# Kernel tuning notes

Hardware: AMD Instinct MI355X
Metric: run time of the kernel (lower is better)

The kernel has to match this reference:

```python
import jax, jax.numpy as jnp
import numpy as np

B, TQ, TV, D, U = 16, 64, 256, 512, 512

def setup_inputs() -> dict:
    key = jax.random.key(0)
    ks = jax.random.split(key, 9)
    s = 1.0 / np.sqrt(D)
    return {
        "query": jax.random.normal(ks[0], (B, TQ, D), dtype=jnp.float32),
        "values": jax.random.normal(ks[1], (B, TV, D), dtype=jnp.float32),
        "enc_mask": jax.random.randint(ks[2], (B, TV), 0, 2, dtype=jnp.int32),
        "W1": jax.random.normal(ks[3], (D, U), dtype=jnp.float32) * s,
        "b1": jnp.zeros((U,), dtype=jnp.float32),
        "W2": jax.random.normal(ks[4], (D, U), dtype=jnp.float32) * s,
        "b2": jnp.zeros((U,), dtype=jnp.float32),
        "Vw": jax.random.normal(ks[5], (U,), dtype=jnp.float32) * (1.0 / np.sqrt(U)),
        "Vb": jnp.zeros((), dtype=jnp.float32),
    }

def reference(query, values, enc_mask, W1, b1, W2, b2, Vw, Vb):
    # q_proj: [B,Tq,U]; v_proj: [B,Tv,U]
    q_proj = jnp.einsum("bqd,du->bqu", query, W1) + b1
    v_proj = jnp.einsum("bvd,du->bvu", values, W2) + b2
    # broadcast add -> [B,Tq,Tv,U], tanh, project to scalar score [B,Tq,Tv]
    s = jnp.tanh(q_proj[:, :, None, :] + v_proj[:, None, :, :])
    score = jnp.einsum("bqvu,u->bqv", s, Vw) + Vb
    # additive mask over encoder positions (mask[1] in the original call)
    score = score - (1.0 - enc_mask.astype(score.dtype))[:, None, :] * 1e9
    attn_weights = jax.nn.softmax(score, axis=2)  # [B,Tq,Tv]
    context = jnp.einsum("bqv,bvd->bqd", attn_weights, values)
    return (context, attn_weights)
```

## Files before the change

### kernel.cpp

```cpp
#include <hip/hip_runtime.h>

#define NB  16
#define NTQ 64
#define NTV 256
#define ND  512
#define NU  512

typedef _Float16 half8_t __attribute__((ext_vector_type(8)));
typedef _Float16 half4_t __attribute__((ext_vector_type(4)));
typedef _Float16 half2_t __attribute__((ext_vector_type(2)));
typedef float floatx4 __attribute__((ext_vector_type(4)));

#if __has_builtin(__builtin_amdgcn_fdot2)
#define FDOT2(a, b, c) __builtin_amdgcn_fdot2((a), (b), (c), false)
#else
#define FDOT2(a, b, c) ((c) + (float)((a)[0]) * (float)((b)[0]) + (float)((a)[1]) * (float)((b)[1]))
#endif
#if __has_builtin(__builtin_amdgcn_rcph)
#define RCPH(x) ((_Float16)__builtin_amdgcn_rcph((_Float16)(x)))
#else
#define RCPH(x) ((_Float16)__builtin_amdgcn_rcpf((float)(x)))
#endif

__device__ __forceinline__ float wred_sum(float x) {
#pragma unroll
    for (int m = 1; m < 64; m <<= 1) x += __shfl_xor(x, m, 64);
    return x;
}
__device__ __forceinline__ float wred_max(float x) {
#pragma unroll
    for (int m = 1; m < 64; m <<= 1) x = fmaxf(x, __shfl_xor(x, m, 64));
    return x;
}

__global__ __launch_bounds__(256) void prep_kernel(
        const float* __restrict__ W1, const float* __restrict__ W2,
        _Float16* __restrict__ W1T, _Float16* __restrict__ W2T) {
    const int blk = blockIdx.x;
    const int t = threadIdx.x;
    __shared__ float tb[32][33];
    const float* W = (blk < 256) ? W1 : W2;
    _Float16* WT = (blk < 256) ? W1T : W2T;
    const int tile = blk & 255;
    const int tr = tile >> 4, tc = tile & 15;
    const int c = t & 31, r8 = t >> 5;
#pragma unroll
    for (int i = 0; i < 4; ++i) {
        int r = r8 + 8 * i;
        tb[r][c] = W[(tr * 32 + r) * 512 + tc * 32 + c];
    }
    __syncthreads();
#pragma unroll
    for (int i = 0; i < 4; ++i) {
        int r = r8 + 8 * i;
        WT[(tc * 32 + r) * 512 + tr * 32 + c] = (_Float16)tb[c][r];
    }
}

__global__ __launch_bounds__(256, 2) void proj_gemm_kernel(
        const float* __restrict__ query, const float* __restrict__ values,
        const _Float16* __restrict__ W1T, const _Float16* __restrict__ W2T,
        const float* __restrict__ b1, const float* __restrict__ b2,
        _Float16* __restrict__ Eqh, _Float16* __restrict__ Evp) {
    __shared__ __align__(16) _Float16 As[2][32 * 40];
    __shared__ __align__(16) _Float16 Bs[2][128 * 40];
    const float KC = 2.8853900817779268f;
    const int bid = blockIdx.x;
    const int t = threadIdx.x;
    const int l = t & 63, w = t >> 6;

    const float* Agf; const _Float16* Bg; const float* bias; _Float16* Cg;
    int mt, nt;
    if (bid < 128) {
        mt = bid >> 2; nt = bid & 3;
        Agf = query; Bg = W1T; bias = b1; Cg = Eqh;
    } else {
        const int vb = bid - 128;
        mt = vb >> 2; nt = vb & 3;
        Agf = values; Bg = W2T; bias = b2; Cg = Evp;
    }
    const int tm = mt * 32, tn = nt * 128;

    const int arow = t >> 3, acol = (t & 7) * 4;
    const int brow = t >> 1, bcol = (t & 1) * 16;
    const float* aptr = Agf + (tm + arow) * 512 + acol;
    const _Float16* bptr = Bg + (tn + brow) * 512 + bcol;

    const int wm = (w & 1) * 16, wn = (w >> 1) * 64;
    const int lr = l & 15, lk = l >> 4;

    floatx4 acc[4] = {};
    float4 fX, fY; half8_t hX0, hX1, hY0, hY1;

#define LOAD_X(kk) do { fX = *(const float4*)(aptr + (kk) * 32); \
        hX0 = *(const half8_t*)(bptr + (kk) * 32); \
        hX1 = *(const half8_t*)(bptr + (kk) * 32 + 8); } while (0)
#define LOAD_Y(kk) do { fY = *(const float4*)(aptr + (kk) * 32); \
        hY0 = *(const half8_t*)(bptr + (kk) * 32); \
        hY1 = *(const half8_t*)(bptr + (kk) * 32 + 8); } while (0)
#define STORE_X(buf) do { \
        half4_t h = {(_Float16)fX.x, (_Float16)fX.y, (_Float16)fX.z, (_Float16)fX.w}; \
        *(half4_t*)(As[buf] + arow * 40 + acol) = h; \
        *(half8_t*)(Bs[buf] + brow * 40 + bcol) = hX0; \
        *(half8_t*)(Bs[buf] + brow * 40 + bcol + 8) = hX1; } while (0)
#define STORE_Y(buf) do { \
        half4_t h = {(_Float16)fY.x, (_Float16)fY.y, (_Float16)fY.z, (_Float16)fY.w}; \
        *(half4_t*)(As[buf] + arow * 40 + acol) = h; \
        *(half8_t*)(Bs[buf] + brow * 40 + bcol) = hY0; \
        *(half8_t*)(Bs[buf] + brow * 40 + bcol + 8) = hY1; } while (0)
#define COMPUTE(buf) do { \
        half8_t af = *(const half8_t*)(As[buf] + (wm + lr) * 40 + lk * 8); \
        half8_t bf0 = *(const half8_t*)(Bs[buf] + (wn + lr) * 40 + lk * 8); \
        half8_t bf1 = *(const half8_t*)(Bs[buf] + (wn + 16 + lr) * 40 + lk * 8); \
        half8_t bf2 = *(const half8_t*)(Bs[buf] + (wn + 32 + lr) * 40 + lk * 8); \
        half8_t bf3 = *(const half8_t*)(Bs[buf] + (wn + 48 + lr) * 40 + lk * 8); \
        acc[0] = __builtin_amdgcn_mfma_f32_16x16x32_f16(af, bf0, acc[0], 0, 0, 0); \
        acc[1] = __builtin_amdgcn_mfma_f32_16x16x32_f16(af, bf1, acc[1], 0, 0, 0); \
        acc[2] = __builtin_amdgcn_mfma_f32_16x16x32_f16(af, bf2, acc[2], 0, 0, 0); \
        acc[3] = __builtin_amdgcn_mfma_f32_16x16x32_f16(af, bf3, acc[3], 0, 0, 0); } while (0)

    LOAD_X(0);
    LOAD_Y(1);
    STORE_X(0);
    __syncthreads();

#pragma unroll 1
    for (int k2 = 0; k2 < 16; k2 += 2) {
        if (k2 + 2 < 16) LOAD_X(k2 + 2);
        COMPUTE(0);
        STORE_Y(1);
        __syncthreads();
        if (k2 + 3 < 16) LOAD_Y(k2 + 3);
        COMPUTE(1);
        if (k2 + 2 < 16) STORE_X(0);
        __syncthreads();
    }

#pragma unroll
    for (int j = 0; j < 4; ++j) {
        const int gr0 = tm + wm + lk * 4;
        const int gc = tn + wn + 16 * j + lr;
        const float bv = bias[gc];
#pragma unroll
        for (int r = 0; r < 4; ++r) {
            const float e = __builtin_amdgcn_exp2f(KC * (acc[j][r] + bv));
            Cg[(gr0 + r) * NU + gc] = (_Float16)fminf(e, 60000.f);
        }
    }
#undef LOAD_X
#undef LOAD_Y
#undef STORE_X
#undef STORE_Y
#undef COMPUTE
}

__global__ __launch_bounds__(1024) void score_ctx_kernel(
        const _Float16* __restrict__ Eqh, const _Float16* __restrict__ Evp,
        const float* __restrict__ Vw, const int* __restrict__ enc_mask,
        const float* __restrict__ values, float* __restrict__ out) {
    const int bid = blockIdx.x;
    const int b = bid & 15, qp = bid >> 4;
    const int q0 = qp * 2;
    const int t = threadIdx.x;
    const int w = t >> 6, l = t & 63;

    __shared__ float scL8[2][256][9];
    __shared__ float attL[2][256];
    __shared__ float ctxp[2][8][516];
    __shared__ float rs[2][4], ss[2][4];

    {
        const half8_t eqA = *(const half8_t*)(Eqh + (b * NTQ + q0) * NU + l * 8);
        const half8_t eqB = *(const half8_t*)(Eqh + (b * NTQ + q0 + 1) * NU + l * 8);
        const float4 vwf0 = *(const float4*)(Vw + l * 8);
        const float4 vwf1 = *(const float4*)(Vw + l * 8 + 4);
        const half2_t eA0 = {eqA[0], eqA[1]}, eA1 = {eqA[2], eqA[3]},
                      eA2 = {eqA[4], eqA[5]}, eA3 = {eqA[6], eqA[7]};
        const half2_t eB0 = {eqB[0], eqB[1]}, eB1 = {eqB[2], eqB[3]},
                      eB2 = {eqB[4], eqB[5]}, eB3 = {eqB[6], eqB[7]};
        const half2_t w0 = {(_Float16)vwf0.x, (_Float16)vwf0.y},
                      w1 = {(_Float16)vwf0.z, (_Float16)vwf0.w},
                      w2 = {(_Float16)vwf1.x, (_Float16)vwf1.y},
                      w3 = {(_Float16)vwf1.z, (_Float16)vwf1.w};
        const half2_t one2 = {(_Float16)1.0f, (_Float16)1.0f};

        const int mv = (l < 16) ? enc_mask[b * NTV + w * 16 + l] : 0;
        const unsigned long long mbits = __ballot(mv != 0);

        const _Float16* evb = Evp + (b * NTV + w * 16) * NU + l * 8;
#pragma unroll 4
        for (int r = 0; r < 16; ++r) {
            if ((mbits >> r) & 1ull) {
                const half8_t ev8 = *(const half8_t*)(evb + r * NU);
                const half2_t v0 = {ev8[0], ev8[1]}, v1 = {ev8[2], ev8[3]},
                              v2 = {ev8[4], ev8[5]}, v3 = {ev8[6], ev8[7]};
                const half2_t pA0 = eA0 * v0 + one2, pA1 = eA1 * v1 + one2;
                const half2_t pA2 = eA2 * v2 + one2, pA3 = eA3 * v3 + one2;
                const half2_t pB0 = eB0 * v0 + one2, pB1 = eB1 * v1 + one2;
                const half2_t pB2 = eB2 * v2 + one2, pB3 = eB3 * v3 + one2;
                const half2_t rA0 = {RCPH(pA0[0]), RCPH(pA0[1])};
                const half2_t rB0 = {RCPH(pB0[0]), RCPH(pB0[1])};
                const half2_t rA1 = {RCPH(pA1[0]), RCPH(pA1[1])};
                const half2_t rB1 = {RCPH(pB1[0]), RCPH(pB1[1])};
                const half2_t rA2 = {RCPH(pA2[0]), RCPH(pA2[1])};
                const half2_t rB2 = {RCPH(pB2[0]), RCPH(pB2[1])};
                const half2_t rA3 = {RCPH(pA3[0]), RCPH(pA3[1])};
                const half2_t rB3 = {RCPH(pB3[0]), RCPH(pB3[1])};
                float aA = FDOT2(w0, rA0, 0.f);
                float aB = FDOT2(w0, rB0, 0.f);
                aA = FDOT2(w1, rA1, aA);
                aB = FDOT2(w1, rB1, aB);
                float cA = FDOT2(w2, rA2, 0.f);
                float cB = FDOT2(w2, rB2, 0.f);
                cA = FDOT2(w3, rA3, cA);
                cB = FDOT2(w3, rB3, cB);
                float xA = aA + cA, xB = aB + cB;
                xA += __shfl_xor(xA, 32, 64);
                xB += __shfl_xor(xB, 32, 64);
                xA += __shfl_xor(xA, 16, 64);
                xB += __shfl_xor(xB, 16, 64);
                xA += __shfl_xor(xA, 8, 64);
                xB += __shfl_xor(xB, 8, 64);
                if (l < 8) {
                    scL8[0][w * 16 + r][l] = xA;
                    scL8[1][w * 16 + r][l] = xB;
                }
            } else if (l < 8) {
                scL8[0][w * 16 + r][l] = 0.f;
                scL8[1][w * 16 + r][l] = 0.f;
            }
        }
    }
    __syncthreads();

    if (t < 512) {
        const int q = t >> 8, v = t & 255;
        const int w4 = (t >> 6) & 3;
        float s = 0.f;
#pragma unroll
        for (int i = 0; i < 8; ++i) s += scL8[q][v][i];
        float sc = -2.f * s;
        sc -= enc_mask[b * NTV + v] ? 0.f : 1e9f;
        float m = wred_max(sc);
        if (l == 0) rs[q][w4] = m;
        __syncthreads();
        m = fmaxf(fmaxf(rs[q][0], rs[q][1]), fmaxf(rs[q][2], rs[q][3]));
        const float LOG2E = 1.4426950408889634f;
        const float ee = __builtin_amdgcn_exp2f((sc - m) * LOG2E);
        float t0 = wred_sum(ee);
        if (l == 0) ss[q][w4] = t0;
        __syncthreads();
        const float S = (ss[q][0] + ss[q][1]) + (ss[q][2] + ss[q][3]);
        const float a = ee * __builtin_amdgcn_rcpf(S);
        attL[q][v] = a;
        float* out_attn = out + NB * NTQ * ND;
        out_attn[(b * NTQ + q0 + q) * NTV + v] = a;
    } else {
        __syncthreads();
        __syncthreads();
    }
    __syncthreads();

    {
        const int vg = t >> 7;
        const int dq = t & 127;
        const unsigned long long mb2 = __ballot(enc_mask[b * NTV + vg * 32 + l] != 0);
        const float* vsrc = values + (b * NTV + vg * 32) * ND + dq * 4;
        floatx4 c0 = {0.f, 0.f, 0.f, 0.f}, c1 = {0.f, 0.f, 0.f, 0.f};
#pragma unroll 4
        for (int vi = 0; vi < 32; ++vi) {
            if ((mb2 >> vi) & 1ull) {
                const floatx4 vv = *(const floatx4*)(vsrc + vi * ND);
                const int v = vg * 32 + vi;
                const float aw0 = attL[0][v], aw1 = attL[1][v];
#pragma unroll
                for (int j = 0; j < 4; ++j) {
                    c0[j] = fmaf(aw0, vv[j], c0[j]);
                    c1[j] = fmaf(aw1, vv[j], c1[j]);
                }
            }
        }
        *(floatx4*)&ctxp[0][vg][dq * 4] = c0;
        *(floatx4*)&ctxp[1][vg][dq * 4] = c1;
    }
    __syncthreads();
    {
        const int cq = t >> 9, d = t & 511;
        float s = ((ctxp[cq][0][d] + ctxp[cq][1][d]) + (ctxp[cq][2][d] + ctxp[cq][3][d]))
                + ((ctxp[cq][4][d] + ctxp[cq][5][d]) + (ctxp[cq][6][d] + ctxp[cq][7][d]));
        out[(b * NTQ + q0 + cq) * ND + d] = s;
    }
}

extern "C" void kernel_launch(void* const* d_in, const int* in_sizes, int n_in,
                              void* d_out, int out_size, void* d_ws, size_t ws_size,
                              hipStream_t stream) {
    const float* query  = (const float*)d_in[0];
    const float* values = (const float*)d_in[1];
    const int*   emask  = (const int*)d_in[2];
    const float* W1     = (const float*)d_in[3];
    const float* b1     = (const float*)d_in[4];
    const float* W2     = (const float*)d_in[5];
    const float* b2     = (const float*)d_in[6];
    const float* Vw     = (const float*)d_in[7];
    float* out = (float*)d_out;

    char* ws = (char*)d_ws;
    _Float16* W1T = (_Float16*)(ws + 0);
    _Float16* W2T = (_Float16*)(ws + 524288);
    _Float16* Eqh = (_Float16*)(ws + 6291456);
    _Float16* Evp = (_Float16*)(ws + 7340032);

    prep_kernel<<<dim3(512), dim3(256), 0, stream>>>(W1, W2, W1T, W2T);
    proj_gemm_kernel<<<dim3(640), dim3(256), 0, stream>>>(query, values, W1T, W2T,
                                                          b1, b2, Eqh, Evp);
    score_ctx_kernel<<<dim3(512), dim3(1024), 0, stream>>>(Eqh, Evp, Vw, emask, values, out);
}
```

Baseline: 44.57 us.

## Stage values as fp16 for context pass and widen GEMM K-tile to 64

The prep kernel gains 1024 extra blocks that convert the fp32 values tensor to fp16 in workspace. The score/context kernel then reads fp16 values, halving the bytes it loads from memory. Separately, the projection GEMM moves from a K-step of 32 to 64 per shared-memory stage, which halves the number of barrier iterations but enlarges the LDS footprint. The extra conversion pass adds a full read and write of values before the GEMM, and fp16 values reduce context precision.

```diff
diff --git a/kernel.cpp b/kernel.cpp
--- a/kernel.cpp
+++ b/kernel.cpp
@@ -35,25 +35,39 @@
 
 __global__ __launch_bounds__(256) void prep_kernel(
         const float* __restrict__ W1, const float* __restrict__ W2,
-        _Float16* __restrict__ W1T, _Float16* __restrict__ W2T) {
+        const float* __restrict__ values,
+        _Float16* __restrict__ W1T, _Float16* __restrict__ W2T,
+        _Float16* __restrict__ vh) {
     const int blk = blockIdx.x;
     const int t = threadIdx.x;
     __shared__ float tb[32][33];
-    const float* W = (blk < 256) ? W1 : W2;
-    _Float16* WT = (blk < 256) ? W1T : W2T;
-    const int tile = blk & 255;
-    const int tr = tile >> 4, tc = tile & 15;
-    const int c = t & 31, r8 = t >> 5;
-#pragma unroll
-    for (int i = 0; i < 4; ++i) {
-        int r = r8 + 8 * i;
-        tb[r][c] = W[(tr * 32 + r) * 512 + tc * 32 + c];
-    }
-    __syncthreads();
-#pragma unroll
-    for (int i = 0; i < 4; ++i) {
-        int r = r8 + 8 * i;
-        WT[(tc * 32 + r) * 512 + tr * 32 + c] = (_Float16)tb[c][r];
+    if (blk < 512) {
+        const float* W = (blk < 256) ? W1 : W2;
+        _Float16* WT = (blk < 256) ? W1T : W2T;
+        const int tile = blk & 255;
+        const int tr = tile >> 4, tc = tile & 15;
+        const int c = t & 31, r8 = t >> 5;
+#pragma unroll
+        for (int i = 0; i < 4; ++i) {
+            int r = r8 + 8 * i;
+            tb[r][c] = W[(tr * 32 + r) * 512 + tc * 32 + c];
+        }
+        __syncthreads();
+#pragma unroll
+        for (int i = 0; i < 4; ++i) {
+            int r = r8 + 8 * i;
+            WT[(tc * 32 + r) * 512 + tr * 32 + c] = (_Float16)tb[c][r];
+        }
+    } else {
+        const int base = (blk - 512) * 2048 + t * 8;
+        float4 f0 = *(const float4*)(values + base);
+        float4 f1 = *(const float4*)(values + base + 4);
+        half8_t h;
+        h[0] = (_Float16)f0.x; h[1] = (_Float16)f0.y;
+        h[2] = (_Float16)f0.z; h[3] = (_Float16)f0.w;
+        h[4] = (_Float16)f1.x; h[5] = (_Float16)f1.y;
+        h[6] = (_Float16)f1.z; h[7] = (_Float16)f1.w;
+        *(half8_t*)(vh + base) = h;
     }
 }
 
@@ -62,8 +76,8 @@
         const _Float16* __restrict__ W1T, const _Float16* __restrict__ W2T,
         const float* __restrict__ b1, const float* __restrict__ b2,
         _Float16* __restrict__ Eqh, _Float16* __restrict__ Evp) {
-    __shared__ __align__(16) _Float16 As[2][32 * 40];
-    __shared__ __align__(16) _Float16 Bs[2][128 * 40];
+    __shared__ __align__(16) _Float16 As[2][32 * 72];
+    __shared__ __align__(16) _Float16 Bs[2][128 * 72];
     const float KC = 2.8853900817779268f;
     const int bid = blockIdx.x;
     const int t = threadIdx.x;
@@ -81,8 +95,8 @@
     }
     const int tm = mt * 32, tn = nt * 128;
 
-    const int arow = t >> 3, acol = (t & 7) * 4;
-    const int brow = t >> 1, bcol = (t & 1) * 16;
+    const int arow = t >> 3, acol = (t & 7) * 8;
+    const int brow = t >> 1, bcol = (t & 1) * 32;
     const float* aptr = Agf + (tm + arow) * 512 + acol;
     const _Float16* bptr = Bg + (tn + brow) * 512 + bcol;
 
@@ -90,49 +104,46 @@
     const int lr = l & 15, lk = l >> 4;
 
     floatx4 acc[4] = {};
-    float4 fX, fY; half8_t hX0, hX1, hY0, hY1;
-
-#define LOAD_X(kk) do { fX = *(const float4*)(aptr + (kk) * 32); \
-        hX0 = *(const half8_t*)(bptr + (kk) * 32); \
-        hX1 = *(const half8_t*)(bptr + (kk) * 32 + 8); } while (0)
-#define LOAD_Y(kk) do { fY = *(const float4*)(aptr + (kk) * 32); \
-        hY0 = *(const half8_t*)(bptr + (kk) * 32); \
-        hY1 = *(const half8_t*)(bptr + (kk) * 32 + 8); } while (0)
-#define STORE_X(buf) do { \
-        half4_t h = {(_Float16)fX.x, (_Float16)fX.y, (_Float16)fX.z, (_Float16)fX.w}; \
-        *(half4_t*)(As[buf] + arow * 40 + acol) = h; \
-        *(half8_t*)(Bs[buf] + brow * 40 + bcol) = hX0; \
-        *(half8_t*)(Bs[buf] + brow * 40 + bcol + 8) = hX1; } while (0)
-#define STORE_Y(buf) do { \
-        half4_t h = {(_Float16)fY.x, (_Float16)fY.y, (_Float16)fY.z, (_Float16)fY.w}; \
-        *(half4_t*)(As[buf] + arow * 40 + acol) = h; \
-        *(half8_t*)(Bs[buf] + brow * 40 + bcol) = hY0; \
-        *(half8_t*)(Bs[buf] + brow * 40 + bcol + 8) = hY1; } while (0)
-#define COMPUTE(buf) do { \
-        half8_t af = *(const half8_t*)(As[buf] + (wm + lr) * 40 + lk * 8); \
-        half8_t bf0 = *(const half8_t*)(Bs[buf] + (wn + lr) * 40 + lk * 8); \
-        half8_t bf1 = *(const half8_t*)(Bs[buf] + (wn + 16 + lr) * 40 + lk * 8); \
-        half8_t bf2 = *(const half8_t*)(Bs[buf] + (wn + 32 + lr) * 40 + lk * 8); \
-        half8_t bf3 = *(const half8_t*)(Bs[buf] + (wn + 48 + lr) * 40 + lk * 8); \
+    float4 aX0, aX1; half8_t bX0, bX1, bX2, bX3;
+
+#define LOADK(kk) do { \
+        const float* ap = aptr + (kk) * 64; \
+        aX0 = *(const float4*)ap; aX1 = *(const float4*)(ap + 4); \
+        const _Float16* bp = bptr + (kk) * 64; \
+        bX0 = *(const half8_t*)bp;        bX1 = *(const half8_t*)(bp + 8); \
+        bX2 = *(const half8_t*)(bp + 16); bX3 = *(const half8_t*)(bp + 24); \
+    } while (0)
+#define STOREK(buf) do { \
+        half8_t h = {(_Float16)aX0.x, (_Float16)aX0.y, (_Float16)aX0.z, (_Float16)aX0.w, \
+                     (_Float16)aX1.x, (_Float16)aX1.y, (_Float16)aX1.z, (_Float16)aX1.w}; \
+        *(half8_t*)(As[buf] + arow * 72 + acol) = h; \
+        *(half8_t*)(Bs[buf] + brow * 72 + bcol)      = bX0; \
+        *(half8_t*)(Bs[buf] + brow * 72 + bcol + 8)  = bX1; \
+        *(half8_t*)(Bs[buf] + brow * 72 + bcol + 16) = bX2; \
+        *(half8_t*)(Bs[buf] + brow * 72 + bcol + 24) = bX3; \
+    } while (0)
+#define COMPUTE(buf, koff) do { \
+        half8_t af = *(const half8_t*)(As[buf] + (wm + lr) * 72 + (koff) + lk * 8); \
+        half8_t bf0 = *(const half8_t*)(Bs[buf] + (wn + lr) * 72 + (koff) + lk * 8); \
+        half8_t bf1 = *(const half8_t*)(Bs[buf] + (wn + 16 + lr) * 72 + (koff) + lk * 8); \
+        half8_t bf2 = *(const half8_t*)(Bs[buf] + (wn + 32 + lr) * 72 + (koff) + lk * 8); \
+        half8_t bf3 = *(const half8_t*)(Bs[buf] + (wn + 48 + lr) * 72 + (koff) + lk * 8); \
         acc[0] = __builtin_amdgcn_mfma_f32_16x16x32_f16(af, bf0, acc[0], 0, 0, 0); \
         acc[1] = __builtin_amdgcn_mfma_f32_16x16x32_f16(af, bf1, acc[1], 0, 0, 0); \
         acc[2] = __builtin_amdgcn_mfma_f32_16x16x32_f16(af, bf2, acc[2], 0, 0, 0); \
         acc[3] = __builtin_amdgcn_mfma_f32_16x16x32_f16(af, bf3, acc[3], 0, 0, 0); } while (0)
 
-    LOAD_X(0);
-    LOAD_Y(1);
-    STORE_X(0);
+    LOADK(0);
+    STOREK(0);
     __syncthreads();
 
 #pragma unroll 1
-    for (int k2 = 0; k2 < 16; k2 += 2) {
-        if (k2 + 2 < 16) LOAD_X(k2 + 2);
-        COMPUTE(0);
-        STORE_Y(1);
-        __syncthreads();
-        if (k2 + 3 < 16) LOAD_Y(k2 + 3);
-        COMPUTE(1);
-        if (k2 + 2 < 16) STORE_X(0);
+    for (int kk = 0; kk < 8; ++kk) {
+        const int cur = kk & 1;
+        if (kk < 7) LOADK(kk + 1);
+        COMPUTE(cur, 0);
+        COMPUTE(cur, 32);
+        if (kk < 7) STOREK(cur ^ 1);
         __syncthreads();
     }
 
@@ -147,17 +158,15 @@
             Cg[(gr0 + r) * NU + gc] = (_Float16)fminf(e, 60000.f);
         }
     }
-#undef LOAD_X
-#undef LOAD_Y
-#undef STORE_X
-#undef STORE_Y
+#undef LOADK
+#undef STOREK
 #undef COMPUTE
 }
 
 __global__ __launch_bounds__(1024) void score_ctx_kernel(
         const _Float16* __restrict__ Eqh, const _Float16* __restrict__ Evp,
         const float* __restrict__ Vw, const int* __restrict__ enc_mask,
-        const float* __restrict__ values, float* __restrict__ out) {
+        const _Float16* __restrict__ vh, float* __restrict__ out) {
     const int bid = blockIdx.x;
     const int b = bid & 15, qp = bid >> 4;
     const int q0 = qp * 2;
@@ -265,12 +274,13 @@
         const int vg = t >> 7;
         const int dq = t & 127;
         const unsigned long long mb2 = __ballot(enc_mask[b * NTV + vg * 32 + l] != 0);
-        const float* vsrc = values + (b * NTV + vg * 32) * ND + dq * 4;
+        const _Float16* vsrc = vh + (b * NTV + vg * 32) * ND + dq * 4;
         floatx4 c0 = {0.f, 0.f, 0.f, 0.f}, c1 = {0.f, 0.f, 0.f, 0.f};
 #pragma unroll 4
         for (int vi = 0; vi < 32; ++vi) {
             if ((mb2 >> vi) & 1ull) {
-                const floatx4 vv = *(const floatx4*)(vsrc + vi * ND);
+                const half4_t vvh = *(const half4_t*)(vsrc + vi * ND);
+                const floatx4 vv = {(float)vvh[0], (float)vvh[1], (float)vvh[2], (float)vvh[3]};
                 const int v = vg * 32 + vi;
                 const float aw0 = attL[0][v], aw1 = attL[1][v];
 #pragma unroll
@@ -308,11 +318,12 @@
     char* ws = (char*)d_ws;
     _Float16* W1T = (_Float16*)(ws + 0);
     _Float16* W2T = (_Float16*)(ws + 524288);
+    _Float16* vh  = (_Float16*)(ws + 2097152);
     _Float16* Eqh = (_Float16*)(ws + 6291456);
     _Float16* Evp = (_Float16*)(ws + 7340032);
 
-    prep_kernel<<<dim3(512), dim3(256), 0, stream>>>(W1, W2, W1T, W2T);
+    prep_kernel<<<dim3(1536), dim3(256), 0, stream>>>(W1, W2, values, W1T, W2T, vh);
     proj_gemm_kernel<<<dim3(640), dim3(256), 0, stream>>>(query, values, W1T, W2T,
                                                           b1, b2, Eqh, Evp);
-    score_ctx_kernel<<<dim3(512), dim3(1024), 0, stream>>>(Eqh, Evp, Vw, emask, values, out);
-}
+    score_ctx_kernel<<<dim3(512), dim3(1024), 0, stream>>>(Eqh, Evp, Vw, emask, vh, out);
+}
```

After: 43.26 us, median of 3. 1.03x faster.
